# Optimization experiments

Measured on AMD Instinct MI355X. Metric: run time of the kernel, lower is better.

The kernel has to match this reference:

```python
import jax, jax.numpy as jnp
import numpy as np

N_DIMS = 1024
N_HEADS = 16
HEAD_DIM = N_DIMS // N_HEADS


def setup_inputs() -> dict:
    key = jax.random.key(0)
    k_x, k_wa, k_wp = jax.random.split(key, 3)
    x = jax.random.normal(k_x, (4, 2048, N_DIMS), dtype=jnp.float32)
    # nn.Linear weights stored [out, in]; apply as x @ W.T
    scale_a = 1.0 / np.sqrt(N_DIMS)
    w_attn = jax.random.uniform(k_wa, (3 * N_DIMS, N_DIMS), jnp.float32, -scale_a, scale_a)
    w_proj = jax.random.uniform(k_wp, (N_DIMS, N_DIMS), jnp.float32, -scale_a, scale_a)
    return {"x": x, "w_attn": w_attn, "w_proj": w_proj}


def reference(x, w_attn, w_proj):
    B, S, D = x.shape
    qkv = x @ w_attn.T                                  # [B, S, 3D]
    q, k, v = jnp.split(qkv, 3, axis=-1)
    # [B, H, S, Dh]
    def heads(t):
        return t.reshape(B, S, N_HEADS, HEAD_DIM).transpose(0, 2, 1, 3)
    q, k, v = heads(q), heads(k), heads(v)
    scores = jnp.einsum('bhqd,bhkd->bhqk', q, k) * (1.0 / np.sqrt(HEAD_DIM))
    causal = jnp.tril(jnp.ones((S, S), dtype=bool))
    scores = jnp.where(causal[None, None], scores, -jnp.inf)
    attn = jax.nn.softmax(scores, axis=-1)              # dropout: eval mode (identity)
    y = jnp.einsum('bhqk,bhkd->bhqd', attn, v)
    y = y.transpose(0, 2, 1, 3).reshape(B, S, D)
    return y @ w_proj.T
```

## Files before the change

kernel.cpp:

```cpp
#include <hip/hip_runtime.h>

typedef unsigned short ushort_t;
typedef __attribute__((ext_vector_type(8))) short bf16x8;
typedef __attribute__((ext_vector_type(4))) float f32x4;


__device__ __forceinline__ ushort_t f2bf(float f) {
    union { float f; unsigned u; } c; c.f = f;
    unsigned u = c.u;
    unsigned r = (u + 0x7fffu + ((u >> 16) & 1u)) >> 16;
    return (ushort_t)r;
}

__device__ __forceinline__ unsigned pk_bf16(float a, float b) {
    unsigned r;
    asm("v_cvt_pk_bf16_f32 %0, %1, %2" : "=v"(r) : "v"(a), "v"(b));
    return r;
}

__device__ __forceinline__ void gld_lds16(const ushort_t* g, ushort_t* l) {
    __builtin_amdgcn_global_load_lds(
        (const __attribute__((address_space(1))) void*)g,
        (__attribute__((address_space(3))) void*)l, 16, 0, 0);
}


__global__ __launch_bounds__(256) void convert_all(
    const float* __restrict__ x, const float* __restrict__ wa, const float* __restrict__ wp,
    ushort_t* __restrict__ xb, ushort_t* __restrict__ wab, ushort_t* __restrict__ wpb)
{
    const int i = blockIdx.x * blockDim.x + threadIdx.x;
    const float* src; ushort_t* dst; int j;
    if (i < 2097152)      { src = x;  dst = xb;  j = i; }
    else if (i < 2883584) { src = wa; dst = wab; j = i - 2097152; }
    else                  { src = wp; dst = wpb; j = i - 2883584; }
    const float4 f = ((const float4*)src)[j];
    ushort4 o;
    o.x = f2bf(f.x); o.y = f2bf(f.y); o.z = f2bf(f.z); o.w = f2bf(f.w);
    ((ushort4*)dst)[j] = o;
}


__global__ __launch_bounds__(256, 3) void gemm_qkv(
    const ushort_t* __restrict__ A, const ushort_t* __restrict__ W,
    ushort_t* __restrict__ qo, ushort_t* __restrict__ ko, ushort_t* __restrict__ vto)
{
    constexpr int K = 1024;
    const int m0 = blockIdx.x * 128;
    const int n0 = blockIdx.y * 128;
    __shared__ alignas(16) ushort_t smem[16384];
    ushort_t* sA = smem;
    ushort_t* sB = smem + 8192;
    const int tid = threadIdx.x;
    const int wave = tid >> 6, lane = tid & 63;
    const int quad = lane >> 4, l16 = lane & 15;
    const int l8 = lane & 7;
    const int wm = (wave >> 1) << 6, wn = (wave & 1) << 6;
    const int srow8 = lane >> 3;
    const int sg = ((l8 ^ srow8) << 3);

    f32x4 acc[4][4] = {};
    const ushort_t* aRow0 = A + (size_t)(m0 + wave * 32 + srow8) * K + sg;
    const ushort_t* bRow0 = W + (size_t)(n0 + wave * 32 + srow8) * K + sg;

    for (int k0 = 0; k0 < K; k0 += 64) {
#pragma unroll
        for (int c = 0; c < 4; ++c) {
            gld_lds16(aRow0 + (size_t)c * 8 * K + k0, sA + (wave * 4 + c) * 512);
            gld_lds16(bRow0 + (size_t)c * 8 * K + k0, sB + (wave * 4 + c) * 512);
        }
        __syncthreads();
#pragma unroll
        for (int ks = 0; ks < 2; ++ks) {
            const int rg = (((ks * 4 + quad) ^ l8) << 3);
            bf16x8 bfr[4];
#pragma unroll
            for (int nf = 0; nf < 4; ++nf)
                bfr[nf] = *(const bf16x8*)(sB + (wn + nf * 16 + l16) * 64 + rg);
#pragma unroll
            for (int mf = 0; mf < 4; ++mf) {
                const bf16x8 af = *(const bf16x8*)(sA + (wm + mf * 16 + l16) * 64 + rg);
#pragma unroll
                for (int nf = 0; nf < 4; ++nf)
                    acc[mf][nf] = __builtin_amdgcn_mfma_f32_16x16x32_bf16(af, bfr[nf], acc[mf][nf], 0, 0, 0);
            }
        }
        __syncthreads();
    }

    const int which = n0 >> 10;
    ushort_t* sT = smem + wave * 2048;
    const int b  = (m0 + wm) >> 11;
    const int sb = (m0 + wm) & 2047;
    const int h  = ((n0 + wn) & 1023) >> 6;
    const int bh = b * 16 + h;

    if (which < 2) {
        ushort_t* go = (which == 0) ? qo : ko;
        const float qs1 = (which == 0) ? 0.18033688011112042f : 1.0f;
#pragma unroll
        for (int mf = 0; mf < 4; ++mf) {
#pragma unroll
            for (int nf = 0; nf < 4; ++nf)
#pragma unroll
                for (int i = 0; i < 4; ++i) {
                    const int mll = quad * 4 + i;
                    sT[mll * 64 + ((nf * 16 + l16) ^ (4 * (mll & 7)))] = f2bf(acc[mf][nf][i] * qs1);
                }
            __builtin_amdgcn_s_waitcnt(0);
#pragma unroll
            for (int p = 0; p < 4; ++p) {
                const int mll = p * 4 + quad;
                const ushort4 val = *(const ushort4*)(sT + mll * 64 + ((l16 * 4) ^ (4 * (mll & 7))));
                const int s = sb + mf * 16 + mll;
                *(ushort4*)(go + ((size_t)bh * 2048 + s) * 64 + l16 * 4) = val;
            }
            __builtin_amdgcn_s_waitcnt(0);
        }
    } else {
#pragma unroll
        for (int nf = 0; nf < 4; ++nf) {
#pragma unroll
            for (int mf = 0; mf < 4; ++mf) {
                ushort4 w;
                w.x = f2bf(acc[mf][nf][0]);
                w.y = f2bf(acc[mf][nf][1]);
                w.z = f2bf(acc[mf][nf][2]);
                w.w = f2bf(acc[mf][nf][3]);
                *(ushort4*)(sT + l16 * 64 + ((mf * 16 + quad * 4) ^ (4 * (l16 & 7)))) = w;
            }
            __builtin_amdgcn_s_waitcnt(0);
#pragma unroll
            for (int p = 0; p < 4; ++p) {
                const int nll = p * 4 + quad;
                const ushort4 val = *(const ushort4*)(sT + nll * 64 + ((l16 * 4) ^ (4 * (nll & 7))));
                const int dh = nf * 16 + nll;
                *(ushort4*)(vto + ((size_t)bh * 64 + dh) * 2048 + sb + l16 * 4) = val;
            }
            __builtin_amdgcn_s_waitcnt(0);
        }
    }
}


__global__ __launch_bounds__(512) void attn(
    const ushort_t* __restrict__ qg_, const ushort_t* __restrict__ kg_,
    const ushort_t* __restrict__ vg_, ushort_t* __restrict__ y)
{
    const int bh = blockIdx.x;
    const int b = bh >> 4, h = bh & 15;
    const int tid = threadIdx.x, wave = tid >> 6, lane = tid & 63;
    const int quad = lane >> 4, l16 = lane & 15;
    const int l8 = lane & 7;

    __shared__ alignas(16) ushort_t sQ[8192];
    __shared__ alignas(16) ushort_t sK[4096];
    __shared__ alignas(16) ushort_t sV[4096];

    const ushort_t* kg = kg_ + (size_t)bh * 2048 * 64;
    const ushort_t* vg = vg_ + (size_t)bh * 64 * 2048;

    const int srow8 = lane >> 3;
    const int sg = ((l8 ^ srow8) << 3);

    const int qt = 15 - (int)blockIdx.y;
    const int q0 = qt * 128;
    const int wbase = q0 + wave * 16;
    const int wrow = wbase + l16;

    {
        const ushort_t* qg = qg_ + ((size_t)bh * 2048 + wbase) * 64;
#pragma unroll
        for (int c = 0; c < 2; ++c)
            gld_lds16(qg + (size_t)(c * 8 + srow8) * 64 + sg, sQ + (wave * 2 + c) * 512);
    }
    __builtin_amdgcn_s_waitcnt(0);

    bf16x8 bq[2];
#pragma unroll
    for (int ks = 0; ks < 2; ++ks)
        bq[ks] = *(const bf16x8*)(sQ + (wave * 16 + l16) * 64 + (((ks * 4 + quad) ^ l8) << 3));

    f32x4 oacc[4] = {};
    f32x4 lpv = {0.f, 0.f, 0.f, 0.f};

    const int tmax = 2 * qt + 1;
    for (int t = 0; t <= tmax; ++t) {
        const int k0 = t * 64;
        __syncthreads();
        gld_lds16(kg + (size_t)(k0 + wave * 8 + srow8) * 64 + sg, sK + wave * 512);
        gld_lds16(vg + (size_t)(wave * 8 + srow8) * 2048 + k0 + sg, sV + wave * 512);
        __syncthreads();

        const bool act = (k0 <= wbase + 15);
        if (act) {
            f32x4 sacc[4] = {};
#pragma unroll
            for (int ks = 0; ks < 2; ++ks) {
                bf16x8 ak[4];
#pragma unroll
                for (int kf = 0; kf < 4; ++kf)
                    ak[kf] = *(const bf16x8*)(sK + (kf * 16 + l16) * 64 + (((ks * 4 + quad) ^ l8) << 3));
#pragma unroll
                for (int kf = 0; kf < 4; ++kf)
                    sacc[kf] = __builtin_amdgcn_mfma_f32_16x16x32_bf16(ak[kf], bq[ks], sacc[kf], 0, 0, 0);
            }

            const bool msk = (k0 + 63 > wbase);
            unsigned Xp0[4], Xp1[4];
#pragma unroll
            for (int kf = 0; kf < 4; ++kf) {
                float pv[4];
#pragma unroll
                for (int i = 0; i < 4; ++i) {
                    float sv = sacc[kf][i];
                    if (msk) {
                        const int cg = k0 + kf * 16 + quad * 4 + i;
                        sv = (cg <= wrow) ? sv : -3.0e38f;
                    }
                    pv[i] = __builtin_amdgcn_exp2f(sv);
                    lpv[i] += pv[i];
                }
                Xp0[kf] = pk_bf16(pv[0], pv[1]);
                Xp1[kf] = pk_bf16(pv[2], pv[3]);
            }

            bf16x8 pa[2];
#pragma unroll
            for (int ks = 0; ks < 2; ++ks) {
                unsigned a0 = Xp0[2 * ks], b0 = Xp0[2 * ks + 1];
                asm("v_permlane32_swap_b32 %0, %1" : "+v"(a0), "+v"(b0));
                asm("v_permlane16_swap_b32 %0, %1" : "+v"(a0), "+v"(b0));
                unsigned a1 = Xp1[2 * ks], b1 = Xp1[2 * ks + 1];
                asm("v_permlane32_swap_b32 %0, %1" : "+v"(a1), "+v"(b1));
                asm("v_permlane16_swap_b32 %0, %1" : "+v"(a1), "+v"(b1));
                union { unsigned u4[4]; bf16x8 v; } P;
                P.u4[0] = a0; P.u4[1] = a1; P.u4[2] = b0; P.u4[3] = b1;
                pa[ks] = P.v;
            }

#pragma unroll
            for (int ks = 0; ks < 2; ++ks) {
                const int rgrp = (((ks * 4 + quad) ^ l8) << 3);
                bf16x8 vb[4];
#pragma unroll
                for (int nf = 0; nf < 4; ++nf)
                    vb[nf] = *(const bf16x8*)(sV + (nf * 16 + l16) * 64 + rgrp);
#pragma unroll
                for (int nf = 0; nf < 4; ++nf)
                    oacc[nf] = __builtin_amdgcn_mfma_f32_16x16x32_bf16(pa[ks], vb[nf], oacc[nf], 0, 0, 0);
            }
        }
    }

    float rs = (lpv[0] + lpv[1]) + (lpv[2] + lpv[3]);
    rs += __shfl_xor(rs, 16);
    rs += __shfl_xor(rs, 32);
#pragma unroll
    for (int i = 0; i < 4; ++i) {
        const float inv = 1.0f / __shfl(rs, quad * 4 + i);
        const int r = wbase + quad * 4 + i;
#pragma unroll
        for (int nf = 0; nf < 4; ++nf)
            y[((size_t)b * 2048 + r) * 1024 + h * 64 + nf * 16 + l16] =
                f2bf(oacc[nf][i] * inv);
    }
}


__global__ __launch_bounds__(256, 3) void gemm_proj(
    const ushort_t* __restrict__ A, const ushort_t* __restrict__ W, float* __restrict__ out)
{
    constexpr int K = 1024;
    const int m0 = blockIdx.x * 64;
    const int n0 = blockIdx.y * 128;
    __shared__ alignas(16) ushort_t sA[4096];
    __shared__ alignas(16) ushort_t sB[8192];
    const int tid = threadIdx.x;
    const int wave = tid >> 6, lane = tid & 63;
    const int quad = lane >> 4, l16 = lane & 15;
    const int l8 = lane & 7;
    const int wm = (wave >> 1) << 5;
    const int wn = (wave & 1) << 6;
    const int srow8 = lane >> 3;
    const int sg = ((l8 ^ srow8) << 3);

    f32x4 acc[2][4] = {};
    const ushort_t* aRow0 = A + (size_t)(m0 + wave * 16 + srow8) * K + sg;
    const ushort_t* bRow0 = W + (size_t)(n0 + wave * 32 + srow8) * K + sg;

    for (int k0 = 0; k0 < K; k0 += 64) {
#pragma unroll
        for (int c = 0; c < 2; ++c)
            gld_lds16(aRow0 + (size_t)c * 8 * K + k0, sA + (wave * 2 + c) * 512);
#pragma unroll
        for (int c = 0; c < 4; ++c)
            gld_lds16(bRow0 + (size_t)c * 8 * K + k0, sB + (wave * 4 + c) * 512);
        __syncthreads();
#pragma unroll
        for (int ks = 0; ks < 2; ++ks) {
            const int rg = (((ks * 4 + quad) ^ l8) << 3);
            bf16x8 bfr[4];
#pragma unroll
            for (int nf = 0; nf < 4; ++nf)
                bfr[nf] = *(const bf16x8*)(sB + (wn + nf * 16 + l16) * 64 + rg);
#pragma unroll
            for (int mf = 0; mf < 2; ++mf) {
                const bf16x8 af = *(const bf16x8*)(sA + (wm + mf * 16 + l16) * 64 + rg);
#pragma unroll
                for (int nf = 0; nf < 4; ++nf)
                    acc[mf][nf] = __builtin_amdgcn_mfma_f32_16x16x32_bf16(af, bfr[nf], acc[mf][nf], 0, 0, 0);
            }
        }
        __syncthreads();
    }

#pragma unroll
    for (int mf = 0; mf < 2; ++mf)
#pragma unroll
        for (int nf = 0; nf < 4; ++nf)
#pragma unroll
            for (int i = 0; i < 4; ++i) {
                const int m = m0 + wm + mf * 16 + quad * 4 + i;
                const int n = n0 + wn + nf * 16 + l16;
                out[(size_t)m * 1024 + n] = acc[mf][nf][i];
            }
}


extern "C" void kernel_launch(void* const* d_in, const int* in_sizes, int n_in,
                              void* d_out, int out_size, void* d_ws, size_t ws_size,
                              hipStream_t stream) {
    const float* x  = (const float*)d_in[0];
    const float* wa = (const float*)d_in[1];
    const float* wp = (const float*)d_in[2];
    float* out = (float*)d_out;

    char* ws = (char*)d_ws;
    ushort_t* xb  = (ushort_t*)(ws);
    ushort_t* wab = (ushort_t*)(ws + 16777216);
    ushort_t* wpb = (ushort_t*)(ws + 16777216 + 6291456);
    ushort_t* q   = (ushort_t*)(ws + 25165824);
    ushort_t* k   = (ushort_t*)(ws + 41943040);
    ushort_t* vt  = (ushort_t*)(ws + 58720256);
    ushort_t* y   = xb;

    convert_all<<<12288, 256, 0, stream>>>(x, wa, wp, xb, wab, wpb);

    gemm_qkv<<<dim3(64, 24), 256, 0, stream>>>(xb, wab, q, k, vt);
    attn<<<dim3(64, 16), 512, 0, stream>>>(q, k, vt, y);
    gemm_proj<<<dim3(128, 8), 256, 0, stream>>>(y, wpb, out);
}
```

Baseline: 220.2 us.

## Process two query tiles per wave in attention, halving block threads

The attention kernel now runs 4 waves of 256 threads instead of 8, and each wave handles 32 query rows as two 16-row halves. Each K and V fragment read from shared memory therefore feeds two MFMA streams. Q is loaded straight from global memory into registers, dropping the sQ shared buffer, and each wave loads two K/V chunks per tile. This cuts LDS traffic per unit of work and lets more blocks fit per CU, at the cost of more registers per thread and coarser causal masking granularity per wave.

```diff
diff --git a/kernel.cpp b/kernel.cpp
--- a/kernel.cpp
+++ b/kernel.cpp
@@ -143,7 +143,7 @@
 }
 
 
-__global__ __launch_bounds__(512) void attn(
+__global__ __launch_bounds__(256, 4) void attn(
     const ushort_t* __restrict__ qg_, const ushort_t* __restrict__ kg_,
     const ushort_t* __restrict__ vg_, ushort_t* __restrict__ y)
 {
@@ -153,7 +153,6 @@
     const int quad = lane >> 4, l16 = lane & 15;
     const int l8 = lane & 7;
 
-    __shared__ alignas(16) ushort_t sQ[8192];
     __shared__ alignas(16) ushort_t sK[4096];
     __shared__ alignas(16) ushort_t sV[4096];
 
@@ -165,105 +164,121 @@
 
     const int qt = 15 - (int)blockIdx.y;
     const int q0 = qt * 128;
-    const int wbase = q0 + wave * 16;
-    const int wrow = wbase + l16;
-
-    {
-        const ushort_t* qg = qg_ + ((size_t)bh * 2048 + wbase) * 64;
-#pragma unroll
-        for (int c = 0; c < 2; ++c)
-            gld_lds16(qg + (size_t)(c * 8 + srow8) * 64 + sg, sQ + (wave * 2 + c) * 512);
-    }
-    __builtin_amdgcn_s_waitcnt(0);
-
-    bf16x8 bq[2];
-#pragma unroll
-    for (int ks = 0; ks < 2; ++ks)
-        bq[ks] = *(const bf16x8*)(sQ + (wave * 16 + l16) * 64 + (((ks * 4 + quad) ^ l8) << 3));
-
-    f32x4 oacc[4] = {};
-    f32x4 lpv = {0.f, 0.f, 0.f, 0.f};
+    const int wbase = q0 + wave * 32;
+
+    bf16x8 bq[2][2];
+#pragma unroll
+    for (int qh = 0; qh < 2; ++qh)
+#pragma unroll
+        for (int ks = 0; ks < 2; ++ks)
+            bq[qh][ks] = *(const bf16x8*)(qg_ +
+                ((size_t)bh * 2048 + wbase + qh * 16 + l16) * 64 + ks * 32 + quad * 8);
+
+    f32x4 oacc[2][4] = {};
+    f32x4 lpv[2] = {};
 
     const int tmax = 2 * qt + 1;
     for (int t = 0; t <= tmax; ++t) {
         const int k0 = t * 64;
         __syncthreads();
-        gld_lds16(kg + (size_t)(k0 + wave * 8 + srow8) * 64 + sg, sK + wave * 512);
-        gld_lds16(vg + (size_t)(wave * 8 + srow8) * 2048 + k0 + sg, sV + wave * 512);
-        __syncthreads();
-
-        const bool act = (k0 <= wbase + 15);
-        if (act) {
-            f32x4 sacc[4] = {};
-#pragma unroll
-            for (int ks = 0; ks < 2; ++ks) {
-                bf16x8 ak[4];
-#pragma unroll
-                for (int kf = 0; kf < 4; ++kf)
-                    ak[kf] = *(const bf16x8*)(sK + (kf * 16 + l16) * 64 + (((ks * 4 + quad) ^ l8) << 3));
-#pragma unroll
-                for (int kf = 0; kf < 4; ++kf)
-                    sacc[kf] = __builtin_amdgcn_mfma_f32_16x16x32_bf16(ak[kf], bq[ks], sacc[kf], 0, 0, 0);
-            }
-
-            const bool msk = (k0 + 63 > wbase);
-            unsigned Xp0[4], Xp1[4];
-#pragma unroll
-            for (int kf = 0; kf < 4; ++kf) {
+#pragma unroll
+        for (int c = 0; c < 2; ++c) {
+            const int chunk = wave * 2 + c;
+            gld_lds16(kg + (size_t)(k0 + chunk * 8 + srow8) * 64 + sg, sK + chunk * 512);
+            gld_lds16(vg + (size_t)(chunk * 8 + srow8) * 2048 + k0 + sg, sV + chunk * 512);
+        }
+        __syncthreads();
+
+        const bool act0 = (k0 <= wbase + 15);
+        const bool act1 = (k0 <= wbase + 31);
+        if (!act1) continue;
+
+        unsigned Xp[2][2][4];
+#pragma unroll
+        for (int kf = 0; kf < 4; ++kf) {
+            const bf16x8 ak0 = *(const bf16x8*)(sK + (kf * 16 + l16) * 64 + ((quad ^ l8) << 3));
+            const bf16x8 ak1 = *(const bf16x8*)(sK + (kf * 16 + l16) * 64 + (((4 + quad) ^ l8) << 3));
+            f32x4 s0 = {}, s1 = {};
+            if (act0) {
+                s0 = __builtin_amdgcn_mfma_f32_16x16x32_bf16(ak0, bq[0][0], s0, 0, 0, 0);
+                s0 = __builtin_amdgcn_mfma_f32_16x16x32_bf16(ak1, bq[0][1], s0, 0, 0, 0);
+            }
+            s1 = __builtin_amdgcn_mfma_f32_16x16x32_bf16(ak0, bq[1][0], s1, 0, 0, 0);
+            s1 = __builtin_amdgcn_mfma_f32_16x16x32_bf16(ak1, bq[1][1], s1, 0, 0, 0);
+
+#pragma unroll
+            for (int qh = 0; qh < 2; ++qh) {
+                if (qh == 0 && !act0) continue;
+                const f32x4 sv = (qh == 0) ? s0 : s1;
+                const bool msk = (k0 + 63 > wbase + qh * 16);
+                const int wrow = wbase + qh * 16 + l16;
                 float pv[4];
 #pragma unroll
                 for (int i = 0; i < 4; ++i) {
-                    float sv = sacc[kf][i];
+                    float x = sv[i];
                     if (msk) {
                         const int cg = k0 + kf * 16 + quad * 4 + i;
-                        sv = (cg <= wrow) ? sv : -3.0e38f;
+                        x = (cg <= wrow) ? x : -3.0e38f;
                     }
-                    pv[i] = __builtin_amdgcn_exp2f(sv);
-                    lpv[i] += pv[i];
+                    pv[i] = __builtin_amdgcn_exp2f(x);
                 }
-                Xp0[kf] = pk_bf16(pv[0], pv[1]);
-                Xp1[kf] = pk_bf16(pv[2], pv[3]);
-            }
-
-            bf16x8 pa[2];
+                lpv[qh][0] += pv[0]; lpv[qh][1] += pv[1];
+                lpv[qh][2] += pv[2]; lpv[qh][3] += pv[3];
+                Xp[qh][0][kf] = pk_bf16(pv[0], pv[1]);
+                Xp[qh][1][kf] = pk_bf16(pv[2], pv[3]);
+            }
+        }
+
+        bf16x8 pa[2][2];
+#pragma unroll
+        for (int qh = 0; qh < 2; ++qh) {
+            if (qh == 0 && !act0) continue;
 #pragma unroll
             for (int ks = 0; ks < 2; ++ks) {
-                unsigned a0 = Xp0[2 * ks], b0 = Xp0[2 * ks + 1];
+                unsigned a0 = Xp[qh][0][2 * ks], b0 = Xp[qh][0][2 * ks + 1];
                 asm("v_permlane32_swap_b32 %0, %1" : "+v"(a0), "+v"(b0));
                 asm("v_permlane16_swap_b32 %0, %1" : "+v"(a0), "+v"(b0));
-                unsigned a1 = Xp1[2 * ks], b1 = Xp1[2 * ks + 1];
+                unsigned a1 = Xp[qh][1][2 * ks], b1 = Xp[qh][1][2 * ks + 1];
                 asm("v_permlane32_swap_b32 %0, %1" : "+v"(a1), "+v"(b1));
                 asm("v_permlane16_swap_b32 %0, %1" : "+v"(a1), "+v"(b1));
                 union { unsigned u4[4]; bf16x8 v; } P;
                 P.u4[0] = a0; P.u4[1] = a1; P.u4[2] = b0; P.u4[3] = b1;
-                pa[ks] = P.v;
-            }
-
-#pragma unroll
-            for (int ks = 0; ks < 2; ++ks) {
-                const int rgrp = (((ks * 4 + quad) ^ l8) << 3);
-                bf16x8 vb[4];
+                pa[qh][ks] = P.v;
+            }
+        }
+
+#pragma unroll
+        for (int ks = 0; ks < 2; ++ks) {
+            const int rgrp = (((ks * 4 + quad) ^ l8) << 3);
+            bf16x8 vb[4];
+#pragma unroll
+            for (int nf = 0; nf < 4; ++nf)
+                vb[nf] = *(const bf16x8*)(sV + (nf * 16 + l16) * 64 + rgrp);
+#pragma unroll
+            for (int nf = 0; nf < 4; ++nf)
+                oacc[1][nf] = __builtin_amdgcn_mfma_f32_16x16x32_bf16(pa[1][ks], vb[nf], oacc[1][nf], 0, 0, 0);
+            if (act0) {
 #pragma unroll
                 for (int nf = 0; nf < 4; ++nf)
-                    vb[nf] = *(const bf16x8*)(sV + (nf * 16 + l16) * 64 + rgrp);
-#pragma unroll
-                for (int nf = 0; nf < 4; ++nf)
-                    oacc[nf] = __builtin_amdgcn_mfma_f32_16x16x32_bf16(pa[ks], vb[nf], oacc[nf], 0, 0, 0);
-            }
-        }
-    }
-
-    float rs = (lpv[0] + lpv[1]) + (lpv[2] + lpv[3]);
-    rs += __shfl_xor(rs, 16);
-    rs += __shfl_xor(rs, 32);
-#pragma unroll
-    for (int i = 0; i < 4; ++i) {
-        const float inv = 1.0f / __shfl(rs, quad * 4 + i);
-        const int r = wbase + quad * 4 + i;
-#pragma unroll
-        for (int nf = 0; nf < 4; ++nf)
-            y[((size_t)b * 2048 + r) * 1024 + h * 64 + nf * 16 + l16] =
-                f2bf(oacc[nf][i] * inv);
+                    oacc[0][nf] = __builtin_amdgcn_mfma_f32_16x16x32_bf16(pa[0][ks], vb[nf], oacc[0][nf], 0, 0, 0);
+            }
+        }
+    }
+
+#pragma unroll
+    for (int qh = 0; qh < 2; ++qh) {
+        float rs = (lpv[qh][0] + lpv[qh][1]) + (lpv[qh][2] + lpv[qh][3]);
+        rs += __shfl_xor(rs, 16);
+        rs += __shfl_xor(rs, 32);
+#pragma unroll
+        for (int i = 0; i < 4; ++i) {
+            const float inv = 1.0f / __shfl(rs, quad * 4 + i);
+            const int r = wbase + qh * 16 + quad * 4 + i;
+#pragma unroll
+            for (int nf = 0; nf < 4; ++nf)
+                y[((size_t)b * 2048 + r) * 1024 + h * 64 + nf * 16 + l16] =
+                    f2bf(oacc[qh][nf][i] * inv);
+        }
     }
 }
 
@@ -348,6 +363,6 @@
     convert_all<<<12288, 256, 0, stream>>>(x, wa, wp, xb, wab, wpb);
 
     gemm_qkv<<<dim3(64, 24), 256, 0, stream>>>(xb, wab, q, k, vt);
-    attn<<<dim3(64, 16), 512, 0, stream>>>(q, k, vt, y);
+    attn<<<dim3(64, 16), 256, 0, stream>>>(q, k, vt, y);
     gemm_proj<<<dim3(128, 8), 256, 0, stream>>>(y, wpb, out);
 }
```

After: 233.6 us. 1.06x slower.

## Double-buffer K/V tiles in attention and load Q directly from global

Applied to the files above, without the earlier changes.

The attention loop now keeps two LDS buffers for K and V. The next tile's async global-to-LDS loads are issued right after the barrier, so they overlap with the MFMA work on the current tile, and the loop needs one barrier per iteration instead of two. The Q staging through LDS is dropped: each lane reads its query fragment straight from global memory, which frees that LDS for the second K/V buffer. Correctness depends on the barrier waiting for the outstanding async LDS loads before the buffers are read.

```diff
diff --git a/kernel.cpp b/kernel.cpp
--- a/kernel.cpp
+++ b/kernel.cpp
@@ -153,9 +153,8 @@
     const int quad = lane >> 4, l16 = lane & 15;
     const int l8 = lane & 7;
 
-    __shared__ alignas(16) ushort_t sQ[8192];
-    __shared__ alignas(16) ushort_t sK[4096];
-    __shared__ alignas(16) ushort_t sV[4096];
+    __shared__ alignas(16) ushort_t sK[2][4096];
+    __shared__ alignas(16) ushort_t sV[2][4096];
 
     const ushort_t* kg = kg_ + (size_t)bh * 2048 * 64;
     const ushort_t* vg = vg_ + (size_t)bh * 64 * 2048;
@@ -168,39 +167,41 @@
     const int wbase = q0 + wave * 16;
     const int wrow = wbase + l16;
 
-    {
-        const ushort_t* qg = qg_ + ((size_t)bh * 2048 + wbase) * 64;
-#pragma unroll
-        for (int c = 0; c < 2; ++c)
-            gld_lds16(qg + (size_t)(c * 8 + srow8) * 64 + sg, sQ + (wave * 2 + c) * 512);
-    }
-    __builtin_amdgcn_s_waitcnt(0);
-
     bf16x8 bq[2];
 #pragma unroll
     for (int ks = 0; ks < 2; ++ks)
-        bq[ks] = *(const bf16x8*)(sQ + (wave * 16 + l16) * 64 + (((ks * 4 + quad) ^ l8) << 3));
+        bq[ks] = *(const bf16x8*)(qg_ + ((size_t)bh * 2048 + wrow) * 64 + ks * 32 + quad * 8);
 
     f32x4 oacc[4] = {};
     f32x4 lpv = {0.f, 0.f, 0.f, 0.f};
 
     const int tmax = 2 * qt + 1;
+
+    gld_lds16(kg + (size_t)(wave * 8 + srow8) * 64 + sg, sK[0] + wave * 512);
+    gld_lds16(vg + (size_t)(wave * 8 + srow8) * 2048 + sg, sV[0] + wave * 512);
+
+    int cur = 0;
     for (int t = 0; t <= tmax; ++t) {
+        __syncthreads();
+        if (t < tmax) {
+            const int k0n = (t + 1) * 64;
+            gld_lds16(kg + (size_t)(k0n + wave * 8 + srow8) * 64 + sg, sK[cur ^ 1] + wave * 512);
+            gld_lds16(vg + (size_t)(wave * 8 + srow8) * 2048 + k0n + sg, sV[cur ^ 1] + wave * 512);
+        }
+
         const int k0 = t * 64;
-        __syncthreads();
-        gld_lds16(kg + (size_t)(k0 + wave * 8 + srow8) * 64 + sg, sK + wave * 512);
-        gld_lds16(vg + (size_t)(wave * 8 + srow8) * 2048 + k0 + sg, sV + wave * 512);
-        __syncthreads();
-
         const bool act = (k0 <= wbase + 15);
         if (act) {
+            const ushort_t* sKc = sK[cur];
+            const ushort_t* sVc = sV[cur];
+
             f32x4 sacc[4] = {};
 #pragma unroll
             for (int ks = 0; ks < 2; ++ks) {
                 bf16x8 ak[4];
 #pragma unroll
                 for (int kf = 0; kf < 4; ++kf)
-                    ak[kf] = *(const bf16x8*)(sK + (kf * 16 + l16) * 64 + (((ks * 4 + quad) ^ l8) << 3));
+                    ak[kf] = *(const bf16x8*)(sKc + (kf * 16 + l16) * 64 + (((ks * 4 + quad) ^ l8) << 3));
 #pragma unroll
                 for (int kf = 0; kf < 4; ++kf)
                     sacc[kf] = __builtin_amdgcn_mfma_f32_16x16x32_bf16(ak[kf], bq[ks], sacc[kf], 0, 0, 0);
@@ -245,12 +246,13 @@
                 bf16x8 vb[4];
 #pragma unroll
                 for (int nf = 0; nf < 4; ++nf)
-                    vb[nf] = *(const bf16x8*)(sV + (nf * 16 + l16) * 64 + rgrp);
+                    vb[nf] = *(const bf16x8*)(sVc + (nf * 16 + l16) * 64 + rgrp);
 #pragma unroll
                 for (int nf = 0; nf < 4; ++nf)
                     oacc[nf] = __builtin_amdgcn_mfma_f32_16x16x32_bf16(pa[ks], vb[nf], oacc[nf], 0, 0, 0);
             }
         }
+        cur ^= 1;
     }
 
     float rs = (lpv[0] + lpv[1]) + (lpv[2] + lpv[3]);
```

Result: no change. 220.3 us (+0.1%).
